# Kernel optimization log

Hardware: AMD Instinct MI355X
Metric: run time of the kernel (lower is better)

The kernel has to match this reference:

```python
import jax, jax.numpy as jnp
import numpy as np

LAYER_NORM_EPS = 1e-6
N_HEAD, D_MODEL, D_HEAD = 16, 1024, 64
QLEN, RLEN, BSZ = 2048, 2048, 2


def _rel_shift(x):
    # x: [T, C, b, n] -> Transformer-XL relative shift
    T, C = x.shape[0], x.shape[1]
    tail = x.shape[2:]
    zero_pad = jnp.zeros((T, 1) + tail, dtype=x.dtype)
    x_padded = jnp.concatenate([zero_pad, x], axis=1)          # [T, C+1, b, n]
    x_padded = x_padded.reshape((C + 1, T) + tail)             # [C+1, T, b, n]
    return x_padded[1:].reshape(x.shape)                       # [T, C, b, n]


def _layer_norm(x, gamma, beta):
    mu = jnp.mean(x, axis=-1, keepdims=True)
    var = jnp.mean(jnp.square(x - mu), axis=-1, keepdims=True)
    return (x - mu) * jax.lax.rsqrt(var + LAYER_NORM_EPS) * gamma + beta


def setup_inputs() -> dict:
    key = jax.random.key(0)
    ks = jax.random.split(key, 8)
    s_qkv = 1.0 / np.sqrt(D_MODEL)
    return {
        "h": jax.random.normal(ks[0], (QLEN, BSZ, D_MODEL), jnp.float32),
        "r": jax.random.normal(ks[1], (RLEN, D_MODEL), jnp.float32),
        "r_w_bias": jax.random.normal(ks[2], (N_HEAD, D_HEAD), jnp.float32) * 0.02,
        "r_r_bias": jax.random.normal(ks[3], (N_HEAD, D_HEAD), jnp.float32) * 0.02,
        "W_qkv": jax.random.normal(ks[4], (D_MODEL, 3 * N_HEAD * D_HEAD), jnp.float32) * s_qkv,
        "W_r": jax.random.normal(ks[5], (D_MODEL, N_HEAD * D_HEAD), jnp.float32) * s_qkv,
        "W_o": jax.random.normal(ks[6], (N_HEAD * D_HEAD, D_MODEL), jnp.float32) * s_qkv,
        "ln_gamma": jnp.ones((D_MODEL,), jnp.float32),
        "ln_beta": jnp.zeros((D_MODEL,), jnp.float32),
    }


def reference(h, r, r_w_bias, r_r_bias, W_qkv, W_r, W_o, ln_gamma, ln_beta):
    qlen, bsz = h.shape[0], h.shape[1]
    n_head, d_head = N_HEAD, D_HEAD
    scale = 1.0 / np.sqrt(d_head).astype(np.float32)

    w_heads = h @ W_qkv                                   # [q, b, 3*n*d]
    w_q, w_k, w_v = jnp.split(w_heads, 3, axis=-1)
    r_k = (r @ W_r).reshape(r.shape[0], n_head, d_head)    # [rlen, n, d]

    klen = w_k.shape[0]
    w_q = w_q.reshape(qlen, bsz, n_head, d_head)
    w_k = w_k.reshape(klen, bsz, n_head, d_head)
    w_v = w_v.reshape(klen, bsz, n_head, d_head)

    AC = jnp.einsum('ibnd,jbnd->ijbn', w_q + r_w_bias, w_k)
    BD = jnp.einsum('ibnd,jnd->ijbn', w_q + r_r_bias, r_k)
    BD = _rel_shift(BD)

    attn_score = (AC + BD) * scale                         # [q, k, b, n]
    attn_prob = jax.nn.softmax(attn_score, axis=1)

    attn_vec = jnp.einsum('ijbn,jbnd->ibnd', attn_prob, w_v)
    attn_vec = attn_vec.reshape(qlen, bsz, n_head * d_head)
    attn_out = attn_vec @ W_o                              # [q, b, d_model]

    # post-norm residual (pre_norm=False)
    return _layer_norm(h + attn_out, ln_gamma, ln_beta)
```

## Files before the change

kernel.cpp:

```cpp
#include <hip/hip_runtime.h>
#include <hip/hip_bf16.h>

typedef unsigned short u16;
typedef __attribute__((ext_vector_type(8))) short s16x8;
typedef __attribute__((ext_vector_type(8))) unsigned short u16x8;
typedef __attribute__((ext_vector_type(4))) float f32x4;

#define SEQ 2048
#define KEXP 0.18033688011112042f

__device__ __forceinline__ float bf2f(u16 x) {
  union { unsigned u; float f; } c; c.u = ((unsigned)x) << 16; return c.f;
}
__device__ __forceinline__ u16 f2bf(float f) {
  __hip_bfloat16 h = __float2bfloat16(f);
  return __builtin_bit_cast(u16, h);
}
__device__ __forceinline__ unsigned pack2(float a, float b) {
  return (unsigned)f2bf(a) | ((unsigned)f2bf(b) << 16);
}

__global__ __launch_bounds__(256) void k_cvt(const float* __restrict__ src,
                                             u16* __restrict__ dst, int n4) {
  int i = blockIdx.x * 256 + threadIdx.x;
  if (i >= n4) return;
  float4 v = ((const float4*)src)[i];
  ((ushort4*)dst)[i] = make_ushort4(f2bf(v.x), f2bf(v.y), f2bf(v.z), f2bf(v.w));
}

__global__ __launch_bounds__(256) void k_tcvt(const float* __restrict__ src,
                                              u16* __restrict__ dst, int R, int C) {
  __shared__ u16 T[64][72];
  int r0 = blockIdx.y * 64, c0 = blockIdx.x * 64;
  int tid = threadIdx.x;
#pragma unroll
  for (int p = 0; p < 4; ++p) {
    int f = p * 256 + tid;
    int r = f >> 4, cc = (f & 15) * 4;
    float4 v = *(const float4*)(src + (size_t)(r0 + r) * C + c0 + cc);
    T[r][cc + 0] = f2bf(v.x); T[r][cc + 1] = f2bf(v.y);
    T[r][cc + 2] = f2bf(v.z); T[r][cc + 3] = f2bf(v.w);
  }
  __syncthreads();
#pragma unroll
  for (int p = 0; p < 2; ++p) {
    int f = p * 256 + tid;
    int c = f >> 3, rr = (f & 7) * 8;
    u16x8 v;
#pragma unroll
    for (int e = 0; e < 8; ++e) v[e] = T[rr + e][c];
    *(u16x8*)(dst + (size_t)(c0 + c) * R + r0 + rr) = v;
  }
}

template <int RES>
__global__ __launch_bounds__(256) void k_gemm_bt(const u16* __restrict__ A,
                                                 const u16* __restrict__ Bt,
                                                 u16* __restrict__ Cb,
                                                 float* __restrict__ Cf,
                                                 const float* __restrict__ res,
                                                 int M, int N, int K) {
  __shared__ u16 As[128 * 72];
  __shared__ u16 Bs[128 * 72];
  const int tid = threadIdx.x;
  const int l = tid & 63, wv = tid >> 6;
  const int g = l >> 4, c16 = l & 15;
  const int m0 = blockIdx.x * 128, n0 = blockIdx.y * 128;
  const int wr = (wv >> 1) * 64, wc = (wv & 1) * 64;
  f32x4 acc[4][4] = {};
  for (int k0 = 0; k0 < K; k0 += 64) {
    __syncthreads();
#pragma unroll
    for (int p = 0; p < 4; ++p) {
      int f = p * 256 + tid;
      int row = f >> 3, kb = (f & 7) * 8;
      u16x8 va = *(const u16x8*)(A + (size_t)(m0 + row) * K + k0 + kb);
      u16x8 vb = *(const u16x8*)(Bt + (size_t)(n0 + row) * K + k0 + kb);
      *(u16x8*)&As[row * 72 + kb] = va;
      *(u16x8*)&Bs[row * 72 + kb] = vb;
    }
    __syncthreads();
#pragma unroll
    for (int ks = 0; ks < 2; ++ks) {
      s16x8 af[4], bf[4];
#pragma unroll
      for (int fr = 0; fr < 4; ++fr)
        af[fr] = *(const s16x8*)&As[(wr + fr * 16 + c16) * 72 + ks * 32 + g * 8];
#pragma unroll
      for (int fc = 0; fc < 4; ++fc)
        bf[fc] = *(const s16x8*)&Bs[(wc + fc * 16 + c16) * 72 + ks * 32 + g * 8];
#pragma unroll
      for (int fr = 0; fr < 4; ++fr)
#pragma unroll
        for (int fc = 0; fc < 4; ++fc)
          acc[fr][fc] = __builtin_amdgcn_mfma_f32_16x16x32_bf16(af[fr], bf[fc],
                                                                acc[fr][fc], 0, 0, 0);
    }
  }
#pragma unroll
  for (int fr = 0; fr < 4; ++fr)
#pragma unroll
    for (int fc = 0; fc < 4; ++fc)
#pragma unroll
      for (int reg = 0; reg < 4; ++reg) {
        int row = m0 + wr + fr * 16 + g * 4 + reg;
        int col = n0 + wc + fc * 16 + c16;
        float v = acc[fr][fc][reg];
        if (RES) Cf[(size_t)row * N + col] = v + res[(size_t)row * N + col];
        else     Cb[(size_t)row * N + col] = f2bf(v);
      }
}

__global__ __launch_bounds__(256) void k_vt(const u16* __restrict__ qkv,
                                            u16* __restrict__ vT) {
  __shared__ u16 T[64][72];
  const int tid = threadIdx.x;
  const int j0 = blockIdx.x * 64;
  const int n = blockIdx.y & 15, b = blockIdx.y >> 4;
#pragma unroll
  for (int p = 0; p < 2; ++p) {
    int f = p * 256 + tid;
    int r = f >> 3, cc = (f & 7) * 8;
    *(u16x8*)&T[r][cc] =
        *(const u16x8*)(qkv + ((size_t)((j0 + r) * 2 + b)) * 3072 + 2048 + n * 64 + cc);
  }
  __syncthreads();
#pragma unroll
  for (int p = 0; p < 2; ++p) {
    int f = p * 256 + tid;
    int d = f >> 3, jc = (f & 7) * 8;
    u16x8 v;
#pragma unroll
    for (int e = 0; e < 8; ++e) v[e] = T[jc + e][d];
    *(u16x8*)(vT + ((size_t)((b * 16 + n) * 64 + d)) * 2048 + j0 + jc) = v;
  }
}

__global__ __launch_bounds__(256) void k_attn(const u16* __restrict__ qkv,
                                              const u16* __restrict__ rk,
                                              const u16* __restrict__ vT,
                                              const float* __restrict__ rwb,
                                              const float* __restrict__ rrb,
                                              u16* __restrict__ av) {
  __shared__ u16 Kt[128][72];
  __shared__ u16 Vt[64][136];
  __shared__ u16 St2[65 * 200];
  __shared__ u16 Pt[4][16][136];

  const int tid = threadIdx.x;
  const int l = tid & 63, wv = tid >> 6;
  const int g = l >> 4, c16 = l & 15;
  const int s = blockIdx.x;
  const int y = (s & 7) + 8 * (s >> 8);
  const int x = (s >> 3) & 31;
  const int i0 = x * 64;
  const int n = y & 15, b = y >> 4;
  const int ii = wv * 16 + c16;
  const f32x4 zero4 = {0.f, 0.f, 0.f, 0.f};
  const s16x8 zero8 = {0, 0, 0, 0, 0, 0, 0, 0};

  s16x8 qw[2];
  {
    int i = i0 + wv * 16 + c16;
    const u16* src = qkv + ((size_t)(i * 2 + b)) * 3072 + n * 64;
#pragma unroll
    for (int ks = 0; ks < 2; ++ks) {
      int d0 = ks * 32 + g * 8;
      u16x8 raw = *(const u16x8*)(src + d0);
      u16x8 wq;
#pragma unroll
      for (int e = 0; e < 8; ++e)
        wq[e] = f2bf(bf2f(raw[e]) + rwb[n * 64 + d0 + e]);
      qw[ks] = __builtin_bit_cast(s16x8, wq);
    }
  }
  s16x8 qr_b[4][2];
#pragma unroll
  for (int rb = 0; rb < 4; ++rb) {
    int i = i0 + rb * 16 + c16;
    const u16* src = qkv + ((size_t)(i * 2 + b)) * 3072 + n * 64;
#pragma unroll
    for (int ks = 0; ks < 2; ++ks) {
      int d0 = ks * 32 + g * 8;
      u16x8 raw = *(const u16x8*)(src + d0);
      u16x8 wq;
#pragma unroll
      for (int e = 0; e < 8; ++e)
        wq[e] = f2bf(bf2f(raw[e]) + rrb[n * 64 + d0 + e]);
      qr_b[rb][ks] = __builtin_bit_cast(s16x8, wq);
    }
  }
  s16x8 q64[2];
  {
    int i = i0 + 64; if (i > SEQ - 1) i = SEQ - 1;
    const u16* src = qkv + ((size_t)(i * 2 + b)) * 3072 + n * 64;
#pragma unroll
    for (int ks = 0; ks < 2; ++ks) {
      int d0 = ks * 32 + g * 8;
      u16x8 raw = *(const u16x8*)(src + d0);
      u16x8 wq;
#pragma unroll
      for (int e = 0; e < 8; ++e)
        wq[e] = f2bf(bf2f(raw[e]) + rrb[n * 64 + d0 + e]);
      q64[ks] = __builtin_bit_cast(s16x8, wq);
    }
  }

  u16x8 kpre[4], vpre[4];
  s16x8 rpre[3][2];
  auto issue_loads = [&](int j0n) {
#pragma unroll
    for (int p = 0; p < 4; ++p) {
      int f = p * 256 + tid;
      kpre[p] = *(const u16x8*)(qkv + ((size_t)((j0n + (f >> 3)) * 2 + b)) * 3072 +
                                1024 + n * 64 + (f & 7) * 8);
    }
#pragma unroll
    for (int p = 0; p < 4; ++p) {
      int f = p * 256 + tid;
      vpre[p] = *(const u16x8*)(vT + ((size_t)((b * 16 + n) * 64 + (f >> 4))) * 2048 +
                                j0n + (f & 15) * 8);
    }
#pragma unroll
    for (int c3 = 0; c3 < 3; ++c3) {
      int w = (wv * 3 + c3) * 16 + c16;
      int u = j0n - i0 - 63 + w;
      int c = (u <= 0) ? (u + (SEQ - 1)) : (u - 2);
      const u16* p = rk + (size_t)(c < 0 ? 0 : c) * 1024 + n * 64;
      rpre[c3][0] = *(const s16x8*)(p + g * 8);
      rpre[c3][1] = *(const s16x8*)(p + 32 + g * 8);
      if (c < 0) { rpre[c3][0] = zero8; rpre[c3][1] = zero8; }
    }
  };

  float m_prev = -1e30f, l_sum = 0.f;
  f32x4 o_acc[4];
#pragma unroll
  for (int r = 0; r < 4; ++r) o_acc[r] = zero4;

  issue_loads(0);

  for (int it = 0; it < 16; ++it) {
    const int j0 = it * 128;
    const int wbthr = (64 + i0 - j0) >> 4;
    __syncthreads();

#pragma unroll
    for (int p = 0; p < 4; ++p) {
      int f = p * 256 + tid;
      *(u16x8*)&Kt[f >> 3][(f & 7) * 8] = kpre[p];
    }
#pragma unroll
    for (int p = 0; p < 4; ++p) {
      int f = p * 256 + tid;
      *(u16x8*)&Vt[f >> 4][(f & 15) * 8] = vpre[p];
    }

#pragma unroll
    for (int c3 = 0; c3 < 3; ++c3) {
      const int wb = wv * 3 + c3;
      const int du = (wb >= wbthr) ? 1 : 0;
#pragma unroll
      for (int rb = 0; rb < 4; ++rb) {
        f32x4 q = zero4;
        q = __builtin_amdgcn_mfma_f32_16x16x32_bf16(rpre[c3][0], qr_b[rb][0], q, 0, 0, 0);
        q = __builtin_amdgcn_mfma_f32_16x16x32_bf16(rpre[c3][1], qr_b[rb][1], q, 0, 0, 0);
        uint2 pk;
        pk.x = pack2(q[0], q[1]);
        pk.y = pack2(q[2], q[3]);
        *(uint2*)&St2[(rb * 16 + c16 + 1 - du) * 200 + wb * 16 + g * 4] = pk;
      }
      {
        f32x4 q = zero4;
        q = __builtin_amdgcn_mfma_f32_16x16x32_bf16(rpre[c3][0], q64[0], q, 0, 0, 0);
        q = __builtin_amdgcn_mfma_f32_16x16x32_bf16(rpre[c3][1], q64[1], q, 0, 0, 0);
        if (du && c16 == 0) {
          uint2 pk;
          pk.x = pack2(q[0], q[1]);
          pk.y = pack2(q[2], q[3]);
          *(uint2*)&St2[64 * 200 + wb * 16 + g * 4] = pk;
        }
      }
    }
    __syncthreads();

    f32x4 sc[8];
#pragma unroll
    for (int fj = 0; fj < 8; ++fj) sc[fj] = zero4;
    __builtin_amdgcn_s_setprio(1);
#pragma unroll
    for (int ks = 0; ks < 2; ++ks)
#pragma unroll
      for (int fj = 0; fj < 8; ++fj) {
        s16x8 kf = *(const s16x8*)&Kt[fj * 16 + c16][ks * 32 + g * 8];
        sc[fj] = __builtin_amdgcn_mfma_f32_16x16x32_bf16(kf, qw[ks], sc[fj], 0, 0, 0);
      }
    __builtin_amdgcn_s_setprio(0);

    {
      const u16* Sb = &St2[ii * 199 + 263 + g * 4];
#pragma unroll
      for (int fj = 0; fj < 8; ++fj)
#pragma unroll
        for (int reg = 0; reg < 4; ++reg)
          sc[fj][reg] += bf2f(Sb[fj * 16 + reg]);
    }

    float mt = sc[0][0];
#pragma unroll
    for (int fj = 0; fj < 8; ++fj)
#pragma unroll
      for (int reg = 0; reg < 4; ++reg)
        mt = fmaxf(mt, sc[fj][reg]);
    mt = fmaxf(mt, __shfl_xor(mt, 16));
    mt = fmaxf(mt, __shfl_xor(mt, 32));
    float mn = fmaxf(m_prev, mt);
    float al = __builtin_amdgcn_exp2f((m_prev - mn) * KEXP);
    m_prev = mn;
    float mk = mn * KEXP;
    float rs = 0.f;
#pragma unroll
    for (int fj = 0; fj < 8; ++fj)
#pragma unroll
      for (int reg = 0; reg < 4; ++reg) {
        float p = __builtin_amdgcn_exp2f(fmaf(sc[fj][reg], KEXP, -mk));
        rs += p;
        sc[fj][reg] = p;
      }
    rs += __shfl_xor(rs, 16);
    rs += __shfl_xor(rs, 32);
    l_sum = l_sum * al + rs;

    float al_t[4];
#pragma unroll
    for (int reg = 0; reg < 4; ++reg)
      al_t[reg] = __shfl(al, g * 4 + reg, 64);
#pragma unroll
    for (int fd = 0; fd < 4; ++fd)
#pragma unroll
      for (int reg = 0; reg < 4; ++reg)
        o_acc[fd][reg] *= al_t[reg];

#pragma unroll
    for (int fj = 0; fj < 8; ++fj) {
      uint2 pk;
      pk.x = pack2(sc[fj][0], sc[fj][1]);
      pk.y = pack2(sc[fj][2], sc[fj][3]);
      *(uint2*)&Pt[wv][c16][fj * 16 + g * 4] = pk;
    }

    if (it < 15) issue_loads(j0 + 128);

    __builtin_amdgcn_s_setprio(1);
#pragma unroll
    for (int ks = 0; ks < 4; ++ks) {
      s16x8 pa = *(const s16x8*)&Pt[wv][c16][ks * 32 + g * 8];
#pragma unroll
      for (int fd = 0; fd < 4; ++fd) {
        s16x8 vb = *(const s16x8*)&Vt[fd * 16 + c16][ks * 32 + g * 8];
        o_acc[fd] = __builtin_amdgcn_mfma_f32_16x16x32_bf16(pa, vb, o_acc[fd], 0, 0, 0);
      }
    }
    __builtin_amdgcn_s_setprio(0);
  }

  float linv = 1.0f / l_sum;
  float linv_t[4];
#pragma unroll
  for (int reg = 0; reg < 4; ++reg)
    linv_t[reg] = __shfl(linv, g * 4 + reg, 64);
#pragma unroll
  for (int reg = 0; reg < 4; ++reg) {
    int i = i0 + wv * 16 + g * 4 + reg;
    u16* dst = av + ((size_t)(i * 2 + b)) * 1024 + n * 64;
#pragma unroll
    for (int fd = 0; fd < 4; ++fd)
      dst[fd * 16 + c16] = f2bf(o_acc[fd][reg] * linv_t[reg]);
  }
}

__global__ __launch_bounds__(256) void k_ln(const float* __restrict__ tmp,
                                            const float* __restrict__ gamma,
                                            const float* __restrict__ beta,
                                            float* __restrict__ out) {
  __shared__ float r1[4], r2[4];
  const int row = blockIdx.x, tid = threadIdx.x;
  const float* x = tmp + (size_t)row * 1024;
  float4 v = *(const float4*)(x + tid * 4);
  float s1 = v.x + v.y + v.z + v.w;
  float s2 = v.x * v.x + v.y * v.y + v.z * v.z + v.w * v.w;
#pragma unroll
  for (int off = 1; off < 64; off <<= 1) {
    s1 += __shfl_xor(s1, off, 64);
    s2 += __shfl_xor(s2, off, 64);
  }
  if ((tid & 63) == 0) { r1[tid >> 6] = s1; r2[tid >> 6] = s2; }
  __syncthreads();
  s1 = r1[0] + r1[1] + r1[2] + r1[3];
  s2 = r2[0] + r2[1] + r2[2] + r2[3];
  float mu = s1 * (1.f / 1024.f);
  float var = s2 * (1.f / 1024.f) - mu * mu;
  float rstd = rsqrtf(var + 1e-6f);
  float4 gm = *(const float4*)(gamma + tid * 4);
  float4 bt = *(const float4*)(beta + tid * 4);
  float4 o;
  o.x = (v.x - mu) * rstd * gm.x + bt.x;
  o.y = (v.y - mu) * rstd * gm.y + bt.y;
  o.z = (v.z - mu) * rstd * gm.z + bt.z;
  o.w = (v.w - mu) * rstd * gm.w + bt.w;
  *(float4*)(out + (size_t)row * 1024 + tid * 4) = o;
}

extern "C" void kernel_launch(void* const* d_in, const int* in_sizes, int n_in,
                              void* d_out, int out_size, void* d_ws, size_t ws_size,
                              hipStream_t stream) {
  const float* h    = (const float*)d_in[0];
  const float* r    = (const float*)d_in[1];
  const float* rwb  = (const float*)d_in[2];
  const float* rrb  = (const float*)d_in[3];
  const float* Wqkv = (const float*)d_in[4];
  const float* Wr   = (const float*)d_in[5];
  const float* Wo   = (const float*)d_in[6];
  const float* gam  = (const float*)d_in[7];
  const float* bet  = (const float*)d_in[8];
  float* out = (float*)d_out;

  u16* hb     = (u16*)d_ws;
  u16* Wqkv_t = hb + (size_t)4096 * 1024;
  u16* Wr_t   = Wqkv_t + (size_t)3072 * 1024;
  u16* Wo_t   = Wr_t + (size_t)1024 * 1024;
  u16* rb     = Wo_t + (size_t)1024 * 1024;
  u16* qkv    = rb + (size_t)2048 * 1024;
  u16* rk     = qkv + (size_t)4096 * 3072;
  u16* vT     = rk + (size_t)2048 * 1024;
  u16* av     = vT + (size_t)2 * 16 * 64 * 2048;
  float* tmp  = (float*)(av + (size_t)4096 * 1024);

  k_cvt<<<4096, 256, 0, stream>>>(h, hb, 4096 * 1024 / 4);
  k_cvt<<<2048, 256, 0, stream>>>(r, rb, 2048 * 1024 / 4);
  k_tcvt<<<dim3(48, 16), 256, 0, stream>>>(Wqkv, Wqkv_t, 1024, 3072);
  k_tcvt<<<dim3(16, 16), 256, 0, stream>>>(Wr, Wr_t, 1024, 1024);
  k_tcvt<<<dim3(16, 16), 256, 0, stream>>>(Wo, Wo_t, 1024, 1024);
  k_gemm_bt<0><<<dim3(32, 24), 256, 0, stream>>>(hb, Wqkv_t, qkv, nullptr, nullptr,
                                                 4096, 3072, 1024);
  k_gemm_bt<0><<<dim3(16, 8), 256, 0, stream>>>(rb, Wr_t, rk, nullptr, nullptr,
                                                2048, 1024, 1024);
  k_vt<<<dim3(32, 32), 256, 0, stream>>>(qkv, vT);
  k_attn<<<1024, 256, 0, stream>>>(qkv, rk, vT, rwb, rrb, av);
  k_gemm_bt<1><<<dim3(32, 8), 256, 0, stream>>>(av, Wo_t, nullptr, tmp, h,
                                                4096, 1024, 1024);
  k_ln<<<4096, 256, 0, stream>>>(tmp, gam, bet, out);
}
```

Before: 277.7 us.

## Read K and V fragments directly from global memory instead of LDS staging

Removes the shared-memory K and V tiles and their register prefetch pipeline. Each wave now loads its MFMA operand fragments for K and V straight from global memory (relying on L1/L2 caching), cutting LDS usage and the LDS store step. In exchange, each of the four waves redundantly fetches the same K/V data, and the loads are no longer prefetched one iteration ahead, so global latency is exposed directly before the MFMAs.

New measurement: 465.9 us. +67.8%, slower.

```diff
diff --git a/kernel.cpp b/kernel.cpp
--- a/kernel.cpp
+++ b/kernel.cpp
@@ -142,8 +142,6 @@
                                               const float* __restrict__ rwb,
                                               const float* __restrict__ rrb,
                                               u16* __restrict__ av) {
-  __shared__ u16 Kt[128][72];
-  __shared__ u16 Vt[64][136];
   __shared__ u16 St2[65 * 200];
   __shared__ u16 Pt[4][16][136];
 
@@ -206,21 +204,12 @@
     }
   }
 
-  u16x8 kpre[4], vpre[4];
+  const u16* kbase = qkv + (size_t)b * 3072 + 1024 + n * 64 +
+                     (size_t)c16 * 6144 + g * 8;
+  const u16* vbase = vT + ((size_t)(b * 16 + n) * 64 + c16) * 2048 + g * 8;
+
   s16x8 rpre[3][2];
-  auto issue_loads = [&](int j0n) {
-#pragma unroll
-    for (int p = 0; p < 4; ++p) {
-      int f = p * 256 + tid;
-      kpre[p] = *(const u16x8*)(qkv + ((size_t)((j0n + (f >> 3)) * 2 + b)) * 3072 +
-                                1024 + n * 64 + (f & 7) * 8);
-    }
-#pragma unroll
-    for (int p = 0; p < 4; ++p) {
-      int f = p * 256 + tid;
-      vpre[p] = *(const u16x8*)(vT + ((size_t)((b * 16 + n) * 64 + (f >> 4))) * 2048 +
-                                j0n + (f & 15) * 8);
-    }
+  auto issue_rk = [&](int j0n) {
 #pragma unroll
     for (int c3 = 0; c3 < 3; ++c3) {
       int w = (wv * 3 + c3) * 16 + c16;
@@ -238,23 +227,12 @@
 #pragma unroll
   for (int r = 0; r < 4; ++r) o_acc[r] = zero4;
 
-  issue_loads(0);
+  issue_rk(0);
 
   for (int it = 0; it < 16; ++it) {
     const int j0 = it * 128;
     const int wbthr = (64 + i0 - j0) >> 4;
     __syncthreads();
-
-#pragma unroll
-    for (int p = 0; p < 4; ++p) {
-      int f = p * 256 + tid;
-      *(u16x8*)&Kt[f >> 3][(f & 7) * 8] = kpre[p];
-    }
-#pragma unroll
-    for (int p = 0; p < 4; ++p) {
-      int f = p * 256 + tid;
-      *(u16x8*)&Vt[f >> 4][(f & 15) * 8] = vpre[p];
-    }
 
 #pragma unroll
     for (int c3 = 0; c3 < 3; ++c3) {
@@ -284,6 +262,7 @@
     }
     __syncthreads();
 
+    const u16* kb = kbase + (size_t)j0 * 6144;
     f32x4 sc[8];
 #pragma unroll
     for (int fj = 0; fj < 8; ++fj) sc[fj] = zero4;
@@ -292,7 +271,7 @@
     for (int ks = 0; ks < 2; ++ks)
 #pragma unroll
       for (int fj = 0; fj < 8; ++fj) {
-        s16x8 kf = *(const s16x8*)&Kt[fj * 16 + c16][ks * 32 + g * 8];
+        s16x8 kf = *(const s16x8*)(kb + (size_t)fj * 98304 + ks * 32);
         sc[fj] = __builtin_amdgcn_mfma_f32_16x16x32_bf16(kf, qw[ks], sc[fj], 0, 0, 0);
       }
     __builtin_amdgcn_s_setprio(0);
@@ -349,16 +328,17 @@
       *(uint2*)&Pt[wv][c16][fj * 16 + g * 4] = pk;
     }
 
-    if (it < 15) issue_loads(j0 + 128);
-
+    if (it < 15) issue_rk(j0 + 128);
+
+    const u16* vb = vbase + j0;
     __builtin_amdgcn_s_setprio(1);
 #pragma unroll
     for (int ks = 0; ks < 4; ++ks) {
       s16x8 pa = *(const s16x8*)&Pt[wv][c16][ks * 32 + g * 8];
 #pragma unroll
       for (int fd = 0; fd < 4; ++fd) {
-        s16x8 vb = *(const s16x8*)&Vt[fd * 16 + c16][ks * 32 + g * 8];
-        o_acc[fd] = __builtin_amdgcn_mfma_f32_16x16x32_bf16(pa, vb, o_acc[fd], 0, 0, 0);
+        s16x8 vf = *(const s16x8*)(vb + (size_t)fd * 32768 + ks * 32);
+        o_acc[fd] = __builtin_amdgcn_mfma_f32_16x16x32_bf16(pa, vf, o_acc[fd], 0, 0, 0);
       }
     }
     __builtin_amdgcn_s_setprio(0);
```
